# Optimization experiments

Hardware: AMD Instinct MI355X
Metric: run time of the kernel (lower is better)

## Reference

```python
import jax, jax.numpy as jnp
import numpy as np

N = 50000      # nodes
E = 800000     # edges (avg degree 16)
F_IN = 128     # num_features
H1 = 256       # hidden_dims[0]
H2 = 128       # hidden_dims[1]
D_EMB = 64     # embedding_dim
C_CLS = 2      # num_classes
EPS = 1e-5     # BatchNorm eps


def setup_inputs() -> dict:
    key = jax.random.key(0)
    ks = jax.random.split(key, 24)
    f32 = jnp.float32
    def w(k, shape, scale=0.05):
        return jax.random.normal(k, shape, f32) * scale
    inp = {
        "x": jax.random.normal(ks[0], (N, F_IN), f32),
        "edge_index": jax.random.randint(ks[1], (2, E), 0, N, jnp.int32),
        # input_proj
        "Wp": w(ks[2], (F_IN, H1)), "bp": jnp.zeros((H1,), f32),
        # conv1 (SAGEConv): lin_l (neighbors, with bias), lin_r (root, no bias)
        "W1l": w(ks[3], (F_IN, H1)), "b1l": jnp.zeros((H1,), f32), "W1r": w(ks[4], (F_IN, H1)),
        # bn1 (eval mode, running stats)
        "bn1_g": jnp.ones((H1,), f32), "bn1_b": jnp.zeros((H1,), f32),
        "bn1_m": w(ks[5], (H1,), 0.01), "bn1_v": jnp.ones((H1,), f32) + 0.1 * jax.random.uniform(ks[6], (H1,), f32),
        # skip_proj
        "Wsk": w(ks[7], (H1, H2)), "bsk": jnp.zeros((H2,), f32),
        # conv2
        "W2l": w(ks[8], (H1, H2)), "b2l": jnp.zeros((H2,), f32), "W2r": w(ks[9], (H1, H2)),
        # bn2
        "bn2_g": jnp.ones((H2,), f32), "bn2_b": jnp.zeros((H2,), f32),
        "bn2_m": w(ks[10], (H2,), 0.01), "bn2_v": jnp.ones((H2,), f32) + 0.1 * jax.random.uniform(ks[11], (H2,), f32),
        # conv3
        "W3l": w(ks[12], (H2, D_EMB)), "b3l": jnp.zeros((D_EMB,), f32), "W3r": w(ks[13], (H2, D_EMB)),
        # classifier
        "Wc": w(ks[14], (D_EMB, C_CLS)), "bc": jnp.zeros((C_CLS,), f32),
    }
    return inp


def _sage(h, src, dst, Wl, bl, Wr):
    # mean aggregation of source features into destination nodes
    s = jax.ops.segment_sum(h[src], dst, num_segments=N)        # [N, d]
    cnt = jax.ops.segment_sum(jnp.ones((src.shape[0], 1), h.dtype), dst, num_segments=N)
    mean = s / jnp.maximum(cnt, 1.0)
    return mean @ Wl + bl + h @ Wr


def _bn(h, g, b, m, v):
    return (h - m) * jax.lax.rsqrt(v + EPS) * g + b


def reference(x, edge_index, Wp, bp, W1l, b1l, W1r, bn1_g, bn1_b, bn1_m, bn1_v,
              Wsk, bsk, W2l, b2l, W2r, bn2_g, bn2_b, bn2_m, bn2_v,
              W3l, b3l, W3r, Wc, bc):
    src, dst = edge_index[0], edge_index[1]
    identity = x @ Wp + bp                                # input_proj
    h = _sage(x, src, dst, W1l, b1l, W1r)                 # conv1
    h = jax.nn.relu(_bn(h, bn1_g, bn1_b, bn1_m, bn1_v) + identity)
    # dropout is identity in eval mode
    identity = h @ Wsk + bsk                              # skip_proj
    h = _sage(h, src, dst, W2l, b2l, W2r)                 # conv2
    h = jax.nn.relu(_bn(h, bn2_g, bn2_b, bn2_m, bn2_v) + identity)
    emb = _sage(h, src, dst, W3l, b3l, W3r)               # conv3
    logits = emb @ Wc + bc
    return (logits, emb)
```

## Files before the change

kernel.cpp:

```cpp
#include <hip/hip_runtime.h>

#define NN 50000
#define NE 800000
#define SLN 6250
#define CAP 64
#define BCAP 106496
constexpr float EPSV = 1e-5f;

typedef __attribute__((ext_vector_type(8))) short short8;
typedef __attribute__((ext_vector_type(4))) float f32x4;

__device__ __forceinline__ float bf2f(unsigned short u) {
    return __uint_as_float(((unsigned int)u) << 16);
}
__device__ __forceinline__ unsigned short f2bf(float f) {
    unsigned int x = __float_as_uint(f);
    return (unsigned short)((x + 0x7FFFu + ((x >> 16) & 1u)) >> 16);
}

__global__ __launch_bounds__(256) void k_bin(const int* __restrict__ src,
                                             const int* __restrict__ dst,
                                             int* __restrict__ binCnt,
                                             int2* __restrict__ binBuf) {
    __shared__ int hcnt[8];
    __shared__ int hbase[8];
    int tid = threadIdx.x;
    if (tid < 8) hcnt[tid] = 0;
    __syncthreads();
    int q = blockIdx.x * 256 + tid;
    bool val = q < NE / 4;
    int4 d = make_int4(0, 0, 0, 0), s = make_int4(0, 0, 0, 0);
    int b0 = 0, b1 = 0, b2 = 0, b3 = 0, r0 = 0, r1 = 0, r2 = 0, r3 = 0;
    if (val) {
        d = ((const int4*)dst)[q];
        s = ((const int4*)src)[q];
        b0 = d.x / SLN; r0 = atomicAdd(&hcnt[b0], 1);
        b1 = d.y / SLN; r1 = atomicAdd(&hcnt[b1], 1);
        b2 = d.z / SLN; r2 = atomicAdd(&hcnt[b2], 1);
        b3 = d.w / SLN; r3 = atomicAdd(&hcnt[b3], 1);
    }
    __syncthreads();
    if (tid < 8) hbase[tid] = atomicAdd(&binCnt[tid], hcnt[tid]);
    __syncthreads();
    if (val) {
        binBuf[(size_t)b0 * BCAP + hbase[b0] + r0] = make_int2(d.x, s.x);
        binBuf[(size_t)b1 * BCAP + hbase[b1] + r1] = make_int2(d.y, s.y);
        binBuf[(size_t)b2 * BCAP + hbase[b2] + r2] = make_int2(d.z, s.z);
        binBuf[(size_t)b3 * BCAP + hbase[b3] + r3] = make_int2(d.w, s.w);
    }
}

__global__ __launch_bounds__(256) void k_scatter2(const int2* __restrict__ binBuf,
                                                  const int* __restrict__ binCnt,
                                                  int* __restrict__ cnt,
                                                  int* __restrict__ csr) {
    int bin = blockIdx.x & 7;
    int lb = blockIdx.x >> 3;
    int n = binCnt[bin];
    const int2* buf = binBuf + (size_t)bin * BCAP;
    for (int i = lb * 256 + threadIdx.x; i < n; i += 128 * 256) {
        int2 p = buf[i];
        int slot = atomicAdd(&cnt[p.x], 1);
        csr[p.x * CAP + slot] = p.y;
    }
}

__device__ void prep1_body(int t, const float* Wp, const float* bp, const float* W1l,
                           const float* b1l, const float* W1r, const float* g, const float* b,
                           const float* m, const float* v, unsigned short* Wf, float* c) {
    int lane = t & 63, f = (t >> 6) & 3, kt = (t >> 8) & 7;
    int nb = t >> 11;
    int col = nb * 64 + f * 16 + (lane & 15);
    int k0 = kt * 32 + (lane >> 4) * 8;
    float A = g[col] * rsqrtf(v[col] + EPSV);
    unsigned short* o = Wf + (size_t)t * 8;
    for (int j = 0; j < 8; j++) {
        int k = k0 + j;
        float w;
        if (k < 128) w = W1l[k * 256 + col] * A;
        else         w = W1r[(k - 128) * 256 + col] * A + Wp[(k - 128) * 256 + col];
        o[j] = f2bf(w);
    }
    if (t < 256) {
        float At = g[t] * rsqrtf(v[t] + EPSV);
        c[t] = b1l[t] * At + (b[t] - m[t] * At) + bp[t];
    }
}

__device__ void prep2_body(int t, const float* Wsk, const float* bsk, const float* W2l,
                           const float* b2l, const float* W2r, const float* g, const float* b,
                           const float* m, const float* v, unsigned short* Wf, float* c) {
    int lane = t & 63, f = (t >> 6) & 3, kt = (t >> 8) & 7, nb = t >> 11;
    int col = nb * 64 + f * 16 + (lane & 15);
    int k0 = kt * 32 + (lane >> 4) * 8;
    unsigned short* o = Wf + (size_t)t * 8;
    if (col < 128) {
        float A = g[col] * rsqrtf(v[col] + EPSV);
        for (int j = 0; j < 8; j++) o[j] = f2bf(W2l[(k0 + j) * 128 + col] * A);
    } else {
        int cc = col - 128;
        float A = g[cc] * rsqrtf(v[cc] + EPSV);
        for (int j = 0; j < 8; j++)
            o[j] = f2bf(W2r[(k0 + j) * 128 + cc] * A + Wsk[(k0 + j) * 128 + cc]);
    }
    if (t < 128) {
        float At = g[t] * rsqrtf(v[t] + EPSV);
        c[t] = b2l[t] * At + (b[t] - m[t] * At) + bsk[t];
    }
}

__device__ void prep3_body(int t, const float* W3l, const float* b3l, const float* W3r,
                           unsigned short* Wf, float* c) {
    int lane = t & 63, f = (t >> 6) & 3, kt = (t >> 8) & 3, nb = t >> 10;
    int col = nb * 64 + f * 16 + (lane & 15);
    int k0 = kt * 32 + (lane >> 4) * 8;
    unsigned short* o = Wf + (size_t)t * 8;
    if (col < 64) {
        for (int j = 0; j < 8; j++) o[j] = f2bf(W3l[(k0 + j) * 64 + col]);
    } else {
        int cc = col - 64;
        for (int j = 0; j < 8; j++) o[j] = f2bf(W3r[(k0 + j) * 64 + cc]);
    }
    if (t < 64) c[t] = b3l[t];
}

__global__ void k_prep_fused(const float* x, unsigned short* xcat, int* cnt, int* binCnt,
                             const float* Wp, const float* bp,
                             const float* W1l, const float* b1l, const float* W1r,
                             const float* g1, const float* b1, const float* m1, const float* v1,
                             const float* Wsk, const float* bsk,
                             const float* W2l, const float* b2l, const float* W2r,
                             const float* g2, const float* b2, const float* m2, const float* v2,
                             const float* W3l, const float* b3l, const float* W3r,
                             unsigned short* Wf1, unsigned short* Wf2, unsigned short* Wf3,
                             float* c1, float* c2, float* c3) {
    int bb = blockIdx.x;
    if (bb < 6250) {
        int i = bb * 256 + threadIdx.x;
        if (i < NN / 4) ((int4*)cnt)[i] = make_int4(0, 0, 0, 0);
        if (i < 2) ((int4*)binCnt)[i] = make_int4(0, 0, 0, 0);
        if (i >= NN * 128 / 4) return;
        int r = i >> 5, c4 = (i & 31) * 4;
        float4 v = ((const float4*)x)[i];
        ushort4 u = make_ushort4(f2bf(v.x), f2bf(v.y), f2bf(v.z), f2bf(v.w));
        *(ushort4*)&xcat[(size_t)r * 256 + 128 + c4] = u;
    } else if (bb < 6282) {
        prep1_body((bb - 6250) * 256 + threadIdx.x, Wp, bp, W1l, b1l, W1r, g1, b1, m1, v1, Wf1, c1);
    } else if (bb < 6314) {
        prep2_body((bb - 6282) * 256 + threadIdx.x, Wsk, bsk, W2l, b2l, W2r, g2, b2, m2, v2, Wf2, c2);
    } else {
        prep3_body((bb - 6314) * 256 + threadIdx.x, W3l, b3l, W3r, Wf3, c3);
    }
}

template <int K, int TOTN, bool EPI>
__global__ __launch_bounds__(256) void k_gemm(const unsigned short* __restrict__ A,
                                              const unsigned short* __restrict__ Wf,
                                              const float* __restrict__ bias,
                                              unsigned short* __restrict__ Out) {
    constexpr int KT = K / 32;
    constexpr int NB = TOTN / 64;
    __shared__ unsigned short Bs[K * 64];
    int tid = threadIdx.x;
    int lane = tid & 63, w = tid >> 6;
    int bm = blockIdx.x;

    int r0 = bm * 128 + w * 32;
    int ra0 = r0 + (lane & 15);
    int ra1 = ra0 + 16;
    if (ra0 >= NN) ra0 = NN - 1;
    if (ra1 >= NN) ra1 = NN - 1;
    const unsigned short* ap0 = A + (size_t)ra0 * K + ((lane >> 4) * 8);
    const unsigned short* ap1 = A + (size_t)ra1 * K + ((lane >> 4) * 8);
    short8 afr0[KT], afr1[KT];
#pragma unroll
    for (int kt = 0; kt < KT; kt++) {
        afr0[kt] = *(const short8*)(ap0 + kt * 32);
        afr1[kt] = *(const short8*)(ap1 + kt * 32);
    }

    int rb = r0 + (lane >> 4) * 4;

    for (int nb = 0; nb < NB; nb++) {
        __syncthreads();
        {
            const float4* srcp = (const float4*)(Wf + (size_t)nb * K * 64);
            float4* dsts = (float4*)Bs;
            for (int i = tid; i < K * 8; i += 256) dsts[i] = srcp[i];
        }
        __syncthreads();

        f32x4 acc[2][4];
#pragma unroll
        for (int i = 0; i < 2; i++)
#pragma unroll
            for (int f = 0; f < 4; f++) acc[i][f] = (f32x4){0.f, 0.f, 0.f, 0.f};
#pragma unroll
        for (int kt = 0; kt < KT; kt++) {
#pragma unroll
            for (int f = 0; f < 4; f++) {
                short8 bfr = *(const short8*)&Bs[((kt * 4 + f) * 64 + lane) * 8];
                acc[0][f] = __builtin_amdgcn_mfma_f32_16x16x32_bf16(afr0[kt], bfr, acc[0][f], 0, 0, 0);
                acc[1][f] = __builtin_amdgcn_mfma_f32_16x16x32_bf16(afr1[kt], bfr, acc[1][f], 0, 0, 0);
            }
        }

        int cc = nb * 64 + (lane & 15);
#pragma unroll
        for (int af = 0; af < 2; af++) {
#pragma unroll
            for (int f = 0; f < 4; f++) {
                float bv = EPI ? bias[cc + f * 16] : 0.f;
#pragma unroll
                for (int r = 0; r < 4; r++) {
                    int gr = rb + af * 16 + r;
                    if (gr < NN) {
                        float val = acc[af][f][r];
                        if (EPI) val = fmaxf(val + bv, 0.f);
                        Out[(size_t)gr * TOTN + cc + f * 16] = f2bf(val);
                    }
                }
            }
        }
    }
}


__global__ __launch_bounds__(256) void k_aggx(const int* __restrict__ cnt,
                                              const int* __restrict__ csr,
                                              unsigned short* __restrict__ xcat) {
    int lane = threadIdx.x & 63, wv = threadIdx.x >> 6;
    int node = blockIdx.x * 4 + wv;
    int deg = cnt[node];
    const int* cp = csr + node * CAP;
    int g = lane >> 4, l16 = lane & 15;
    float a[8];
#pragma unroll
    for (int j = 0; j < 8; j++) a[j] = 0.f;
    const unsigned short* base = xcat + 128 + l16 * 8;
    int e = 0;
    for (; e + 16 <= deg; e += 16) {
        int s0 = cp[e + g], s1 = cp[e + 4 + g], s2 = cp[e + 8 + g], s3 = cp[e + 12 + g];
        short8 u0 = *(const short8*)(base + (size_t)s0 * 256);
        short8 u1 = *(const short8*)(base + (size_t)s1 * 256);
        short8 u2 = *(const short8*)(base + (size_t)s2 * 256);
        short8 u3 = *(const short8*)(base + (size_t)s3 * 256);
#pragma unroll
        for (int j = 0; j < 8; j++)
            a[j] += (bf2f(u0[j]) + bf2f(u1[j])) + (bf2f(u2[j]) + bf2f(u3[j]));
    }
    for (; e + 4 <= deg; e += 4) {
        short8 u = *(const short8*)(base + (size_t)cp[e + g] * 256);
#pragma unroll
        for (int j = 0; j < 8; j++) a[j] += bf2f(u[j]);
    }
    if (e + g < deg) {
        short8 u = *(const short8*)(base + (size_t)cp[e + g] * 256);
#pragma unroll
        for (int j = 0; j < 8; j++) a[j] += bf2f(u[j]);
    }
#pragma unroll
    for (int j = 0; j < 8; j++) {
        a[j] += __shfl_xor(a[j], 16);
        a[j] += __shfl_xor(a[j], 32);
    }
    if (lane < 16) {
        float inv = 1.f / (float)max(deg, 1);
        ushort4 o0 = make_ushort4(f2bf(a[0] * inv), f2bf(a[1] * inv), f2bf(a[2] * inv), f2bf(a[3] * inv));
        ushort4 o1 = make_ushort4(f2bf(a[4] * inv), f2bf(a[5] * inv), f2bf(a[6] * inv), f2bf(a[7] * inv));
        *(ushort4*)&xcat[(size_t)node * 256 + l16 * 8] = o0;
        *(ushort4*)&xcat[(size_t)node * 256 + l16 * 8 + 4] = o1;
    }
}

__global__ __launch_bounds__(256) void k_agg2(const unsigned short* __restrict__ G,
                                              const int* __restrict__ cnt,
                                              const int* __restrict__ csr,
                                              const float* __restrict__ c,
                                              unsigned short* __restrict__ h2) {
    int lane = threadIdx.x & 63, wv = threadIdx.x >> 6;
    int node = blockIdx.x * 4 + wv;
    int deg = cnt[node];
    const int* cp = csr + node * CAP;
    int g = lane >> 4, l16 = lane & 15;
    float a[8];
#pragma unroll
    for (int j = 0; j < 8; j++) a[j] = 0.f;
    const unsigned short* base = G + l16 * 8;
    int e = 0;
    for (; e + 16 <= deg; e += 16) {
        int s0 = cp[e + g], s1 = cp[e + 4 + g], s2 = cp[e + 8 + g], s3 = cp[e + 12 + g];
        short8 u0 = *(const short8*)(base + (size_t)s0 * 256);
        short8 u1 = *(const short8*)(base + (size_t)s1 * 256);
        short8 u2 = *(const short8*)(base + (size_t)s2 * 256);
        short8 u3 = *(const short8*)(base + (size_t)s3 * 256);
#pragma unroll
        for (int j = 0; j < 8; j++)
            a[j] += (bf2f(u0[j]) + bf2f(u1[j])) + (bf2f(u2[j]) + bf2f(u3[j]));
    }
    for (; e + 4 <= deg; e += 4) {
        short8 u = *(const short8*)(base + (size_t)cp[e + g] * 256);
#pragma unroll
        for (int j = 0; j < 8; j++) a[j] += bf2f(u[j]);
    }
    if (e + g < deg) {
        short8 u = *(const short8*)(base + (size_t)cp[e + g] * 256);
#pragma unroll
        for (int j = 0; j < 8; j++) a[j] += bf2f(u[j]);
    }
#pragma unroll
    for (int j = 0; j < 8; j++) {
        a[j] += __shfl_xor(a[j], 16);
        a[j] += __shfl_xor(a[j], 32);
    }
    if (lane < 16) {
        float inv = 1.f / (float)max(deg, 1);
        short8 r = *(const short8*)&G[(size_t)node * 256 + 128 + l16 * 8];
        const float* cpb = c + l16 * 8;
        unsigned short o[8];
#pragma unroll
        for (int j = 0; j < 8; j++)
            o[j] = f2bf(fmaxf(a[j] * inv + bf2f(r[j]) + cpb[j], 0.f));
        *(ushort4*)&h2[(size_t)node * 128 + l16 * 8] = *(ushort4*)&o[0];
        *(ushort4*)&h2[(size_t)node * 128 + l16 * 8 + 4] = *(ushort4*)&o[4];
    }
}

__global__ __launch_bounds__(256) void k_agg_final(const unsigned short* __restrict__ G,
                                                   const int* __restrict__ cnt,
                                                   const int* __restrict__ csr,
                                                   const float* __restrict__ c,
                                                   const float* __restrict__ Wc,
                                                   const float* __restrict__ bc,
                                                   float* __restrict__ outbuf) {
    int lane = threadIdx.x & 63, wv = threadIdx.x >> 6;
    int node = blockIdx.x * 4 + wv;
    int deg = cnt[node];
    const int* cp = csr + node * CAP;
    int g = lane >> 3, l8 = lane & 7;
    float a[8];
#pragma unroll
    for (int j = 0; j < 8; j++) a[j] = 0.f;
    const unsigned short* base = G + l8 * 8;
    int e = 0;
    for (; e + 32 <= deg; e += 32) {
        int s0 = cp[e + g], s1 = cp[e + 8 + g], s2 = cp[e + 16 + g], s3 = cp[e + 24 + g];
        short8 u0 = *(const short8*)(base + (size_t)s0 * 128);
        short8 u1 = *(const short8*)(base + (size_t)s1 * 128);
        short8 u2 = *(const short8*)(base + (size_t)s2 * 128);
        short8 u3 = *(const short8*)(base + (size_t)s3 * 128);
#pragma unroll
        for (int j = 0; j < 8; j++)
            a[j] += (bf2f(u0[j]) + bf2f(u1[j])) + (bf2f(u2[j]) + bf2f(u3[j]));
    }
    for (; e + 8 <= deg; e += 8) {
        short8 u = *(const short8*)(base + (size_t)cp[e + g] * 128);
#pragma unroll
        for (int j = 0; j < 8; j++) a[j] += bf2f(u[j]);
    }
    if (e + g < deg) {
        short8 u = *(const short8*)(base + (size_t)cp[e + g] * 128);
#pragma unroll
        for (int j = 0; j < 8; j++) a[j] += bf2f(u[j]);
    }
#pragma unroll
    for (int j = 0; j < 8; j++) {
        a[j] += __shfl_xor(a[j], 8);
        a[j] += __shfl_xor(a[j], 16);
        a[j] += __shfl_xor(a[j], 32);
    }
    float l0 = 0.f, l1 = 0.f;
    if (lane < 8) {
        float inv = 1.f / (float)max(deg, 1);
        short8 r = *(const short8*)&G[(size_t)node * 128 + 64 + l8 * 8];
        const float* cpb = c + l8 * 8;
        float v[8];
#pragma unroll
        for (int j = 0; j < 8; j++) v[j] = a[j] * inv + bf2f(r[j]) + cpb[j];
        float* emb = outbuf + 2 * (size_t)NN;
        *(float4*)&emb[(size_t)node * 64 + l8 * 8] = make_float4(v[0], v[1], v[2], v[3]);
        *(float4*)&emb[(size_t)node * 64 + l8 * 8 + 4] = make_float4(v[4], v[5], v[6], v[7]);
        int c0 = l8 * 8;
#pragma unroll
        for (int j = 0; j < 8; j++) {
            l0 += v[j] * Wc[2 * (c0 + j)];
            l1 += v[j] * Wc[2 * (c0 + j) + 1];
        }
    }
    l0 += __shfl_xor(l0, 1); l1 += __shfl_xor(l1, 1);
    l0 += __shfl_xor(l0, 2); l1 += __shfl_xor(l1, 2);
    l0 += __shfl_xor(l0, 4); l1 += __shfl_xor(l1, 4);
    if (lane == 0) {
        outbuf[(size_t)node * 2 + 0] = l0 + bc[0];
        outbuf[(size_t)node * 2 + 1] = l1 + bc[1];
    }
}

extern "C" void kernel_launch(void* const* d_in, const int* in_sizes, int n_in,
                              void* d_out, int out_size, void* d_ws, size_t ws_size,
                              hipStream_t stream) {
    const float* x    = (const float*)d_in[0];
    const int*   ei   = (const int*)d_in[1];
    const float* Wp   = (const float*)d_in[2];
    const float* bp   = (const float*)d_in[3];
    const float* W1l  = (const float*)d_in[4];
    const float* b1l  = (const float*)d_in[5];
    const float* W1r  = (const float*)d_in[6];
    const float* bn1g = (const float*)d_in[7];
    const float* bn1b = (const float*)d_in[8];
    const float* bn1m = (const float*)d_in[9];
    const float* bn1v = (const float*)d_in[10];
    const float* Wsk  = (const float*)d_in[11];
    const float* bsk  = (const float*)d_in[12];
    const float* W2l  = (const float*)d_in[13];
    const float* b2l  = (const float*)d_in[14];
    const float* W2r  = (const float*)d_in[15];
    const float* bn2g = (const float*)d_in[16];
    const float* bn2b = (const float*)d_in[17];
    const float* bn2m = (const float*)d_in[18];
    const float* bn2v = (const float*)d_in[19];
    const float* W3l  = (const float*)d_in[20];
    const float* b3l  = (const float*)d_in[21];
    const float* W3r  = (const float*)d_in[22];
    const float* Wc   = (const float*)d_in[23];
    const float* bc   = (const float*)d_in[24];

    const int* src = ei;
    const int* dst = ei + NE;

    char* ws = (char*)d_ws;
    size_t o = 0;
    auto alloc = [&](size_t b) -> char* {
        char* p = ws + o;
        o = (o + b + 255) & ~(size_t)255;
        return p;
    };
    int* cnt    = (int*)alloc((size_t)NN * 4);
    int* binCnt = (int*)alloc(64);
    int* csr    = (int*)alloc((size_t)NN * CAP * 4);
    unsigned short* xcat = (unsigned short*)alloc((size_t)NN * 256 * 2);
    unsigned short* h1   = (unsigned short*)alloc((size_t)NN * 256 * 2);
    unsigned short* h2   = (unsigned short*)alloc((size_t)NN * 128 * 2);
    unsigned short* G    = (unsigned short*)alloc((size_t)NN * 256 * 2);
    unsigned short* Wf1  = (unsigned short*)alloc((size_t)256 * 256 * 2);
    unsigned short* Wf2  = (unsigned short*)alloc((size_t)256 * 256 * 2);
    unsigned short* Wf3  = (unsigned short*)alloc((size_t)128 * 128 * 2);
    float* c1 = (float*)alloc(256 * 4);
    float* c2 = (float*)alloc(128 * 4);
    float* c3 = (float*)alloc(64 * 4);
    int2* binBuf = (int2*)G;

    float* outbuf = (float*)d_out;

    k_prep_fused<<<6322, 256, 0, stream>>>(x, xcat, cnt, binCnt,
                                           Wp, bp, W1l, b1l, W1r, bn1g, bn1b, bn1m, bn1v,
                                           Wsk, bsk, W2l, b2l, W2r, bn2g, bn2b, bn2m, bn2v,
                                           W3l, b3l, W3r, Wf1, Wf2, Wf3, c1, c2, c3);

    k_bin<<<782, 256, 0, stream>>>(src, dst, binCnt, binBuf);
    k_scatter2<<<1024, 256, 0, stream>>>(binBuf, binCnt, cnt, csr);

    k_aggx<<<12500, 256, 0, stream>>>(cnt, csr, xcat);
    k_gemm<256, 256, true><<<391, 256, 0, stream>>>(xcat, Wf1, c1, h1);

    k_gemm<256, 256, false><<<391, 256, 0, stream>>>(h1, Wf2, nullptr, G);
    k_agg2<<<12500, 256, 0, stream>>>(G, cnt, csr, c2, h2);

    k_gemm<128, 128, false><<<391, 256, 0, stream>>>(h2, Wf3, nullptr, G);
    k_agg_final<<<12500, 256, 0, stream>>>(G, cnt, csr, c3, Wc, bc, outbuf);
}
```

Measured before the change: 215.1 us.

## Gather neighbor features as 8-bit e5m2 for first two aggregations

The gathered neighbor features for conv1 (x) and conv2 (the projected h1@W2l) are now also stored as 8-bit e5m2-style values (fp16 rounded to its top byte), in separate compact arrays. The aggregation kernels read these with 16-byte loads and 8 lanes per row, halving the bytes pulled through random gathers. The GEMM for conv2 writes its neighbor half in this 8-bit format and its root half as bf16 into a separate buffer. The trade is a large loss of mantissa precision in the aggregated means, plus extra writes and memory for the new buffers.

```diff
diff --git a/kernel.cpp b/kernel.cpp
--- a/kernel.cpp
+++ b/kernel.cpp
@@ -1,4 +1,5 @@
 #include <hip/hip_runtime.h>
+#include <hip/hip_fp16.h>
 
 #define NN 50000
 #define NE 800000
@@ -16,6 +17,23 @@
 __device__ __forceinline__ unsigned short f2bf(float f) {
     unsigned int x = __float_as_uint(f);
     return (unsigned short)((x + 0x7FFFu + ((x >> 16) & 1u)) >> 16);
+}
+__device__ __forceinline__ unsigned char f2e5(float f) {
+    unsigned short h = __half_as_ushort(__float2half(f));
+    unsigned short r = h + 0x7F + ((h >> 8) & 1);
+    return (unsigned char)(r >> 8);
+}
+__device__ __forceinline__ void acc16(float* a, uint4 u) {
+#pragma unroll
+    for (int q = 0; q < 4; q++) {
+        unsigned int x = (q == 0) ? u.x : (q == 1) ? u.y : (q == 2) ? u.z : u.w;
+        unsigned int h01 = ((x << 8) & 0xFF00u) | ((x << 16) & 0xFF000000u);
+        unsigned int h23 = ((x >> 8) & 0xFF00u) | (x & 0xFF000000u);
+        __half2 p01 = *(__half2*)&h01, p23 = *(__half2*)&h23;
+        float2 f01 = __half22float2(p01), f23 = __half22float2(p23);
+        a[q * 4 + 0] += f01.x; a[q * 4 + 1] += f01.y;
+        a[q * 4 + 2] += f23.x; a[q * 4 + 3] += f23.y;
+    }
 }
 
 __global__ __launch_bounds__(256) void k_bin(const int* __restrict__ src,
@@ -124,7 +142,8 @@
     if (t < 64) c[t] = b3l[t];
 }
 
-__global__ void k_prep_fused(const float* x, unsigned short* xcat, int* cnt, int* binCnt,
+__global__ void k_prep_fused(const float* x, unsigned short* xcat, unsigned char* xf8,
+                             int* cnt, int* binCnt,
                              const float* Wp, const float* bp,
                              const float* W1l, const float* b1l, const float* W1r,
                              const float* g1, const float* b1, const float* m1, const float* v1,
@@ -144,6 +163,8 @@
         float4 v = ((const float4*)x)[i];
         ushort4 u = make_ushort4(f2bf(v.x), f2bf(v.y), f2bf(v.z), f2bf(v.w));
         *(ushort4*)&xcat[(size_t)r * 256 + 128 + c4] = u;
+        uchar4 u8 = make_uchar4(f2e5(v.x), f2e5(v.y), f2e5(v.z), f2e5(v.w));
+        *(uchar4*)&xf8[(size_t)r * 128 + c4] = u8;
     } else if (bb < 6282) {
         prep1_body((bb - 6250) * 256 + threadIdx.x, Wp, bp, W1l, b1l, W1r, g1, b1, m1, v1, Wf1, c1);
     } else if (bb < 6314) {
@@ -153,11 +174,12 @@
     }
 }
 
-template <int K, int TOTN, bool EPI>
+template <int K, int TOTN, int MODE>
 __global__ __launch_bounds__(256) void k_gemm(const unsigned short* __restrict__ A,
                                               const unsigned short* __restrict__ Wf,
                                               const float* __restrict__ bias,
-                                              unsigned short* __restrict__ Out) {
+                                              unsigned short* __restrict__ Out,
+                                              unsigned char* __restrict__ Pf8) {
     constexpr int KT = K / 32;
     constexpr int NB = TOTN / 64;
     __shared__ unsigned short Bs[K * 64];
@@ -210,14 +232,20 @@
         for (int af = 0; af < 2; af++) {
 #pragma unroll
             for (int f = 0; f < 4; f++) {
-                float bv = EPI ? bias[cc + f * 16] : 0.f;
+                float bv = (MODE == 1) ? bias[cc + f * 16] : 0.f;
 #pragma unroll
                 for (int r = 0; r < 4; r++) {
                     int gr = rb + af * 16 + r;
                     if (gr < NN) {
                         float val = acc[af][f][r];
-                        if (EPI) val = fmaxf(val + bv, 0.f);
-                        Out[(size_t)gr * TOTN + cc + f * 16] = f2bf(val);
+                        if (MODE == 1) val = fmaxf(val + bv, 0.f);
+                        int col = cc + f * 16;
+                        if (MODE == 2) {
+                            if (col < 128) Pf8[(size_t)gr * 128 + col] = f2e5(val);
+                            else           Out[(size_t)gr * 128 + (col - 128)] = f2bf(val);
+                        } else {
+                            Out[(size_t)gr * TOTN + col] = f2bf(val);
+                        }
                     }
                 }
             }
@@ -228,52 +256,50 @@
 
 __global__ __launch_bounds__(256) void k_aggx(const int* __restrict__ cnt,
                                               const int* __restrict__ csr,
+                                              const unsigned char* __restrict__ xf8,
                                               unsigned short* __restrict__ xcat) {
     int lane = threadIdx.x & 63, wv = threadIdx.x >> 6;
     int node = blockIdx.x * 4 + wv;
     int deg = cnt[node];
     const int* cp = csr + node * CAP;
-    int g = lane >> 4, l16 = lane & 15;
-    float a[8];
-#pragma unroll
-    for (int j = 0; j < 8; j++) a[j] = 0.f;
-    const unsigned short* base = xcat + 128 + l16 * 8;
+    int g = lane >> 3, l8 = lane & 7;
+    float a[16];
+#pragma unroll
+    for (int j = 0; j < 16; j++) a[j] = 0.f;
+    const unsigned char* base = xf8 + l8 * 16;
     int e = 0;
     for (; e + 16 <= deg; e += 16) {
-        int s0 = cp[e + g], s1 = cp[e + 4 + g], s2 = cp[e + 8 + g], s3 = cp[e + 12 + g];
-        short8 u0 = *(const short8*)(base + (size_t)s0 * 256);
-        short8 u1 = *(const short8*)(base + (size_t)s1 * 256);
-        short8 u2 = *(const short8*)(base + (size_t)s2 * 256);
-        short8 u3 = *(const short8*)(base + (size_t)s3 * 256);
-#pragma unroll
-        for (int j = 0; j < 8; j++)
-            a[j] += (bf2f(u0[j]) + bf2f(u1[j])) + (bf2f(u2[j]) + bf2f(u3[j]));
-    }
-    for (; e + 4 <= deg; e += 4) {
-        short8 u = *(const short8*)(base + (size_t)cp[e + g] * 256);
-#pragma unroll
-        for (int j = 0; j < 8; j++) a[j] += bf2f(u[j]);
+        int s0 = cp[e + g], s1 = cp[e + 8 + g];
+        uint4 u0 = *(const uint4*)(base + (size_t)s0 * 128);
+        uint4 u1 = *(const uint4*)(base + (size_t)s1 * 128);
+        acc16(a, u0); acc16(a, u1);
     }
     if (e + g < deg) {
-        short8 u = *(const short8*)(base + (size_t)cp[e + g] * 256);
-#pragma unroll
-        for (int j = 0; j < 8; j++) a[j] += bf2f(u[j]);
-    }
-#pragma unroll
-    for (int j = 0; j < 8; j++) {
+        uint4 u = *(const uint4*)(base + (size_t)cp[e + g] * 128);
+        acc16(a, u);
+    }
+    if (e + 8 + g < deg) {
+        uint4 u = *(const uint4*)(base + (size_t)cp[e + 8 + g] * 128);
+        acc16(a, u);
+    }
+#pragma unroll
+    for (int j = 0; j < 16; j++) {
+        a[j] += __shfl_xor(a[j], 8);
         a[j] += __shfl_xor(a[j], 16);
         a[j] += __shfl_xor(a[j], 32);
     }
-    if (lane < 16) {
+    if (lane < 8) {
         float inv = 1.f / (float)max(deg, 1);
-        ushort4 o0 = make_ushort4(f2bf(a[0] * inv), f2bf(a[1] * inv), f2bf(a[2] * inv), f2bf(a[3] * inv));
-        ushort4 o1 = make_ushort4(f2bf(a[4] * inv), f2bf(a[5] * inv), f2bf(a[6] * inv), f2bf(a[7] * inv));
-        *(ushort4*)&xcat[(size_t)node * 256 + l16 * 8] = o0;
-        *(ushort4*)&xcat[(size_t)node * 256 + l16 * 8 + 4] = o1;
-    }
-}
-
-__global__ __launch_bounds__(256) void k_agg2(const unsigned short* __restrict__ G,
+        unsigned short o[16];
+#pragma unroll
+        for (int j = 0; j < 16; j++) o[j] = f2bf(a[j] * inv);
+        *(short8*)&xcat[(size_t)node * 256 + lane * 16] = *(short8*)&o[0];
+        *(short8*)&xcat[(size_t)node * 256 + lane * 16 + 8] = *(short8*)&o[8];
+    }
+}
+
+__global__ __launch_bounds__(256) void k_agg2(const unsigned char* __restrict__ pf8,
+                                              const unsigned short* __restrict__ r2,
                                               const int* __restrict__ cnt,
                                               const int* __restrict__ csr,
                                               const float* __restrict__ c,
@@ -282,47 +308,46 @@
     int node = blockIdx.x * 4 + wv;
     int deg = cnt[node];
     const int* cp = csr + node * CAP;
-    int g = lane >> 4, l16 = lane & 15;
-    float a[8];
-#pragma unroll
-    for (int j = 0; j < 8; j++) a[j] = 0.f;
-    const unsigned short* base = G + l16 * 8;
+    int g = lane >> 3, l8 = lane & 7;
+    float a[16];
+#pragma unroll
+    for (int j = 0; j < 16; j++) a[j] = 0.f;
+    const unsigned char* base = pf8 + l8 * 16;
     int e = 0;
     for (; e + 16 <= deg; e += 16) {
-        int s0 = cp[e + g], s1 = cp[e + 4 + g], s2 = cp[e + 8 + g], s3 = cp[e + 12 + g];
-        short8 u0 = *(const short8*)(base + (size_t)s0 * 256);
-        short8 u1 = *(const short8*)(base + (size_t)s1 * 256);
-        short8 u2 = *(const short8*)(base + (size_t)s2 * 256);
-        short8 u3 = *(const short8*)(base + (size_t)s3 * 256);
-#pragma unroll
-        for (int j = 0; j < 8; j++)
-            a[j] += (bf2f(u0[j]) + bf2f(u1[j])) + (bf2f(u2[j]) + bf2f(u3[j]));
-    }
-    for (; e + 4 <= deg; e += 4) {
-        short8 u = *(const short8*)(base + (size_t)cp[e + g] * 256);
-#pragma unroll
-        for (int j = 0; j < 8; j++) a[j] += bf2f(u[j]);
+        int s0 = cp[e + g], s1 = cp[e + 8 + g];
+        uint4 u0 = *(const uint4*)(base + (size_t)s0 * 128);
+        uint4 u1 = *(const uint4*)(base + (size_t)s1 * 128);
+        acc16(a, u0); acc16(a, u1);
     }
     if (e + g < deg) {
-        short8 u = *(const short8*)(base + (size_t)cp[e + g] * 256);
-#pragma unroll
-        for (int j = 0; j < 8; j++) a[j] += bf2f(u[j]);
-    }
-#pragma unroll
-    for (int j = 0; j < 8; j++) {
+        uint4 u = *(const uint4*)(base + (size_t)cp[e + g] * 128);
+        acc16(a, u);
+    }
+    if (e + 8 + g < deg) {
+        uint4 u = *(const uint4*)(base + (size_t)cp[e + 8 + g] * 128);
+        acc16(a, u);
+    }
+#pragma unroll
+    for (int j = 0; j < 16; j++) {
+        a[j] += __shfl_xor(a[j], 8);
         a[j] += __shfl_xor(a[j], 16);
         a[j] += __shfl_xor(a[j], 32);
     }
-    if (lane < 16) {
+    if (lane < 8) {
         float inv = 1.f / (float)max(deg, 1);
-        short8 r = *(const short8*)&G[(size_t)node * 256 + 128 + l16 * 8];
-        const float* cpb = c + l16 * 8;
-        unsigned short o[8];
+        short8 rA = *(const short8*)&r2[(size_t)node * 128 + lane * 16];
+        short8 rB = *(const short8*)&r2[(size_t)node * 128 + lane * 16 + 8];
+        const float* cpb = c + lane * 16;
+        unsigned short o[16];
 #pragma unroll
         for (int j = 0; j < 8; j++)
-            o[j] = f2bf(fmaxf(a[j] * inv + bf2f(r[j]) + cpb[j], 0.f));
-        *(ushort4*)&h2[(size_t)node * 128 + l16 * 8] = *(ushort4*)&o[0];
-        *(ushort4*)&h2[(size_t)node * 128 + l16 * 8 + 4] = *(ushort4*)&o[4];
+            o[j] = f2bf(fmaxf(a[j] * inv + bf2f(rA[j]) + cpb[j], 0.f));
+#pragma unroll
+        for (int j = 0; j < 8; j++)
+            o[8 + j] = f2bf(fmaxf(a[8 + j] * inv + bf2f(rB[j]) + cpb[8 + j], 0.f));
+        *(short8*)&h2[(size_t)node * 128 + lane * 16] = *(short8*)&o[0];
+        *(short8*)&h2[(size_t)node * 128 + lane * 16 + 8] = *(short8*)&o[8];
     }
 }
 
@@ -438,21 +463,24 @@
     int* cnt    = (int*)alloc((size_t)NN * 4);
     int* binCnt = (int*)alloc(64);
     int* csr    = (int*)alloc((size_t)NN * CAP * 4);
+    unsigned char*  xf8  = (unsigned char*)alloc((size_t)NN * 128);
     unsigned short* xcat = (unsigned short*)alloc((size_t)NN * 256 * 2);
     unsigned short* h1   = (unsigned short*)alloc((size_t)NN * 256 * 2);
+    unsigned char*  pf8  = (unsigned char*)alloc((size_t)NN * 128);
+    unsigned short* r2   = (unsigned short*)alloc((size_t)NN * 128 * 2);
     unsigned short* h2   = (unsigned short*)alloc((size_t)NN * 128 * 2);
-    unsigned short* G    = (unsigned short*)alloc((size_t)NN * 256 * 2);
+    unsigned short* G3   = (unsigned short*)alloc((size_t)NN * 128 * 2);
     unsigned short* Wf1  = (unsigned short*)alloc((size_t)256 * 256 * 2);
     unsigned short* Wf2  = (unsigned short*)alloc((size_t)256 * 256 * 2);
     unsigned short* Wf3  = (unsigned short*)alloc((size_t)128 * 128 * 2);
     float* c1 = (float*)alloc(256 * 4);
     float* c2 = (float*)alloc(128 * 4);
     float* c3 = (float*)alloc(64 * 4);
-    int2* binBuf = (int2*)G;
+    int2* binBuf = (int2*)G3;
 
     float* outbuf = (float*)d_out;
 
-    k_prep_fused<<<6322, 256, 0, stream>>>(x, xcat, cnt, binCnt,
+    k_prep_fused<<<6322, 256, 0, stream>>>(x, xcat, xf8, cnt, binCnt,
                                            Wp, bp, W1l, b1l, W1r, bn1g, bn1b, bn1m, bn1v,
                                            Wsk, bsk, W2l, b2l, W2r, bn2g, bn2b, bn2m, bn2v,
                                            W3l, b3l, W3r, Wf1, Wf2, Wf3, c1, c2, c3);
@@ -460,12 +488,12 @@
     k_bin<<<782, 256, 0, stream>>>(src, dst, binCnt, binBuf);
     k_scatter2<<<1024, 256, 0, stream>>>(binBuf, binCnt, cnt, csr);
 
-    k_aggx<<<12500, 256, 0, stream>>>(cnt, csr, xcat);
-    k_gemm<256, 256, true><<<391, 256, 0, stream>>>(xcat, Wf1, c1, h1);
-
-    k_gemm<256, 256, false><<<391, 256, 0, stream>>>(h1, Wf2, nullptr, G);
-    k_agg2<<<12500, 256, 0, stream>>>(G, cnt, csr, c2, h2);
-
-    k_gemm<128, 128, false><<<391, 256, 0, stream>>>(h2, Wf3, nullptr, G);
-    k_agg_final<<<12500, 256, 0, stream>>>(G, cnt, csr, c3, Wc, bc, outbuf);
-}
+    k_aggx<<<12500, 256, 0, stream>>>(cnt, csr, xf8, xcat);
+    k_gemm<256, 256, 1><<<391, 256, 0, stream>>>(xcat, Wf1, c1, h1, nullptr);
+
+    k_gemm<256, 256, 2><<<391, 256, 0, stream>>>(h1, Wf2, nullptr, r2, pf8);
+    k_agg2<<<12500, 256, 0, stream>>>(pf8, r2, cnt, csr, c2, h2);
+
+    k_gemm<128, 128, 0><<<391, 256, 0, stream>>>(h2, Wf3, nullptr, G3, nullptr);
+    k_agg_final<<<12500, 256, 0, stream>>>(G3, cnt, csr, c3, Wc, bc, outbuf);
+}
```

After: 210.8 us. 2.0% less time.
